# Performance work log

Hardware: AMD Instinct MI355X
Metric: run time of the kernel (lower is better)

The kernel has to match this reference:

```python
import jax, jax.numpy as jnp
import numpy as np

VOCAB = 10000
EMBED = 100
T = 80
UNITS = 512
B = 4096
RATE = 0.2  # Keras LSTMCell dropout on inputs, 4 gate masks, cached across timesteps


def setup_inputs() -> dict:
    key = jax.random.key(0)
    ks = jax.random.split(key, 10)
    s = 0.05
    return {
        "inputs": jax.random.randint(ks[0], (B, T), 0, VOCAB, dtype=jnp.int32),
        "embed": jax.random.normal(ks[1], (VOCAB, EMBED), dtype=jnp.float32) * s,
        "W0": jax.random.normal(ks[2], (EMBED, 4 * UNITS), dtype=jnp.float32) * s,
        "U0": jax.random.normal(ks[3], (UNITS, 4 * UNITS), dtype=jnp.float32) * s,
        "b0": jnp.zeros((4 * UNITS,), dtype=jnp.float32),
        "W1": jax.random.normal(ks[4], (UNITS, 4 * UNITS), dtype=jnp.float32) * s,
        "U1": jax.random.normal(ks[5], (UNITS, 4 * UNITS), dtype=jnp.float32) * s,
        "b1": jnp.zeros((4 * UNITS,), dtype=jnp.float32),
        "Wout": jax.random.normal(ks[6], (UNITS, 1), dtype=jnp.float32) * s,
        "bout": jnp.zeros((1,), dtype=jnp.float32),
    }


def _dropout_masks(key, shape):
    keep = 1.0 - RATE
    return jax.random.bernoulli(key, keep, shape).astype(jnp.float32) / keep


def _lstm_cell(h, c, xt, masks, W, U, b, in_dim):
    # masks: [4, B, in_dim] per-gate input dropout masks (fixed across time)
    # kernel layout: W.reshape(in_dim, 4, UNITS), gate order i, f, g(cand), o
    z = jnp.einsum('gbd,dgh->bgh', xt[None] * masks, W.reshape(in_dim, 4, UNITS))
    z = z + (h @ U + b).reshape(-1, 4, UNITS)
    i = jax.nn.sigmoid(z[:, 0])
    f = jax.nn.sigmoid(z[:, 1])
    g = jnp.tanh(z[:, 2])
    o = jax.nn.sigmoid(z[:, 3])
    c_new = f * c + i * g
    h_new = o * jnp.tanh(c_new)
    return h_new, c_new


def reference(inputs, embed, W0, U0, b0, W1, U1, b1, Wout, bout):
    x = embed[inputs]                      # [B, T, EMBED]
    mkey = jax.random.key(42)
    k0, k1 = jax.random.split(mkey)
    m0 = _dropout_masks(k0, (4, B, EMBED))
    m1 = _dropout_masks(k1, (4, B, UNITS))

    def step(carry, xt):
        h0, c0, h1, c1 = carry
        h0, c0 = _lstm_cell(h0, c0, xt, m0, W0, U0, b0, EMBED)
        h1, c1 = _lstm_cell(h1, c1, h0, m1, W1, U1, b1, UNITS)
        return (h0, c0, h1, c1), None

    init = tuple(jnp.zeros((B, UNITS), dtype=jnp.float32) for _ in range(4))
    (h0, c0, h1, c1), _ = jax.lax.scan(step, init, jnp.swapaxes(x, 0, 1))
    return jax.nn.sigmoid(h1 @ Wout + bout)   # [B, 1]
```

## Files before the change

### kernel.cpp

```cpp
#include <hip/hip_runtime.h>
#include <hip/hip_bf16.h>
#include <stdint.h>

#define BATCH 4096
#define TT    80
#define EMB   100
#define UNITS 512
#define N4    2048
#define K0P   128

typedef unsigned short ushort;
typedef unsigned char uchar;
typedef __bf16 bf16x8 __attribute__((ext_vector_type(8)));
typedef float f32x4 __attribute__((ext_vector_type(4)));

__device__ __forceinline__ uint32_t rotl32(uint32_t x, uint32_t r) {
  return (x << r) | (x >> (32u - r));
}
__device__ __forceinline__ void tf_round4(uint32_t& x0, uint32_t& x1,
                                          int r0, int r1, int r2, int r3) {
  x0 += x1; x1 = rotl32(x1, r0); x1 ^= x0;
  x0 += x1; x1 = rotl32(x1, r1); x1 ^= x0;
  x0 += x1; x1 = rotl32(x1, r2); x1 ^= x0;
  x0 += x1; x1 = rotl32(x1, r3); x1 ^= x0;
}
__device__ __forceinline__ void tf2x32(uint32_t k0, uint32_t k1,
                                       uint32_t x0, uint32_t x1,
                                       uint32_t& y0, uint32_t& y1) {
  uint32_t k2 = k0 ^ k1 ^ 0x1BD11BDAu;
  x0 += k0; x1 += k1;
  tf_round4(x0, x1, 13, 15, 26, 6);  x0 += k1; x1 += k2 + 1u;
  tf_round4(x0, x1, 17, 29, 16, 24); x0 += k2; x1 += k0 + 2u;
  tf_round4(x0, x1, 13, 15, 26, 6);  x0 += k0; x1 += k1 + 3u;
  tf_round4(x0, x1, 17, 29, 16, 24); x0 += k1; x1 += k2 + 4u;
  tf_round4(x0, x1, 13, 15, 26, 6);  x0 += k2; x1 += k0 + 5u;
  y0 = x0; y1 = x1;
}
__device__ __forceinline__ int keepbit(uint32_t u) {
  float f = __uint_as_float((u >> 9) | 0x3F800000u) - 1.0f;
  return f < 0.8f ? 1 : 0;
}

__device__ __forceinline__ ushort f2bf(float f) {
  uint32_t u = __float_as_uint(f);
  uint32_t r = (u + 0x7FFFu + ((u >> 16) & 1u)) >> 16;
  return (ushort)r;
}
__device__ __forceinline__ float bf2f(ushort u) {
  return __uint_as_float(((uint32_t)u) << 16);
}

#define M0N (4 * BATCH * EMB)
#define M1N (4 * BATCH * UNITS)

__global__ __launch_bounds__(256) void masks_kernel(uchar* __restrict__ m0p,
                                                    uchar* __restrict__ m1p) {
  uint32_t k0a, k0b, k1a, k1b;
  tf2x32(0u, 42u, 0u, 0u, k0a, k0b);
  tf2x32(0u, 42u, 0u, 1u, k1a, k1b);
  const int n0 = BATCH * EMB;
  const int n1 = BATCH * UNITS;
  const int total = n0 + n1;
  for (int i = blockIdx.x * blockDim.x + threadIdx.x; i < total;
       i += gridDim.x * blockDim.x) {
    if (i < n0) {
      uchar byte = 0;
#pragma unroll
      for (int g = 0; g < 4; g++) {
        uint32_t y0, y1;
        tf2x32(k0a, k0b, 0u, (uint32_t)(g * n0 + i), y0, y1);
        byte |= keepbit(y0 ^ y1) << g;
      }
      m0p[i] = byte;
    } else {
      int j = i - n0;
      uchar byte = 0;
#pragma unroll
      for (int g = 0; g < 4; g++) {
        uint32_t y0, y1;
        tf2x32(k1a, k1b, 0u, (uint32_t)(g * n1 + j), y0, y1);
        byte |= keepbit(y0 ^ y1) << g;
      }
      m1p[j] = byte;
    }
  }
}

__global__ __launch_bounds__(256) void convT(const float* __restrict__ src,
                                             ushort* __restrict__ dst,
                                             int Ksrc, int Kpad) {
  __shared__ float t[32][33];
  const int n0 = blockIdx.x * 32, kk0 = blockIdx.y * 32;
  const int tx = threadIdx.x & 31, ty = threadIdx.x >> 5;
#pragma unroll
  for (int r = ty; r < 32; r += 8) {
    const int k = kk0 + r;
    t[r][tx] = (k < Ksrc) ? src[(size_t)k * N4 + n0 + tx] : 0.f;
  }
  __syncthreads();
#pragma unroll
  for (int r = ty; r < 32; r += 8)
    dst[(size_t)(n0 + r) * Kpad + kk0 + tx] = f2bf(t[tx][r]);
}

__device__ __forceinline__ void xm0_prep_one(int i, int t,
                                             const int* __restrict__ inputs,
                                             const float* __restrict__ embed,
                                             const uchar* __restrict__ m0p,
                                             ushort* __restrict__ Xm0) {
  const int k = i & 127;
  const int b = (i >> 7) & 4095;
  const int g = i >> 19;
  float v = 0.f;
  if (k < EMB) {
    const int idx = inputs[b * TT + t];
    const float e = embed[(size_t)idx * EMB + k];
    v = ((m0p[b * EMB + k] >> g) & 1) ? e * 1.25f : 0.f;
  }
  Xm0[((size_t)g << 19) + (b << 7) + k] = f2bf(v);
}

__global__ __launch_bounds__(256) void prep0_kernel(const int* __restrict__ inputs,
                                                    const float* __restrict__ embed,
                                                    const uchar* __restrict__ m0p,
                                                    ushort* __restrict__ Xm0) {
  const int i = blockIdx.x * blockDim.x + threadIdx.x;
  xm0_prep_one(i, 0, inputs, embed, m0p, Xm0);
}

__device__ __forceinline__ void gload16(const void* g, void* l) {
  __builtin_amdgcn_global_load_lds(
      (const __attribute__((address_space(1))) unsigned int*)g,
      (__attribute__((address_space(3))) unsigned int*)l, 16, 0, 0);
}

__global__ __launch_bounds__(256) void cell_gemm_mfma(
    const ushort* __restrict__ A1, int K1,
    const ushort* __restrict__ B1,
    const ushort* __restrict__ A2,
    const ushort* __restrict__ B2,
    const float* __restrict__ bias,
    float* __restrict__ z) {
  __shared__ __align__(16) ushort As[128 * 32];
  __shared__ __align__(16) ushort Bs[128 * 32];

  const int tid = threadIdx.x;
  const int w = tid >> 6, l = tid & 63;
  const int bm0 = blockIdx.x * 128, bn0 = blockIdx.y * 128;
  const int gate = bn0 >> 9;
  const int wm = (w >> 1) * 64, wn = (w & 1) * 64;
  const int fr = l & 15, kq = l >> 4;
  const int schunk = (l & 3) * 8;
  const int srow_l = l >> 2;

  f32x4 acc[4][4] = {};

  const ushort* A1g = A1 + (size_t)gate * BATCH * K1;

#pragma unroll 1
  for (int seg = 0; seg < 2; seg++) {
    const ushort* A = seg ? A2 : A1g;
    const ushort* B = seg ? B2 : B1;
    const int K = seg ? UNITS : K1;
#pragma unroll 1
    for (int k0 = 0; k0 < K; k0 += 32) {
#pragma unroll
      for (int c2 = 0; c2 < 2; c2++) {
        const int r = (w * 2 + c2) * 16 + srow_l;
        gload16(A + (size_t)(bm0 + r) * K + k0 + schunk,
                (void*)(As + (w * 2 + c2) * 512));
        gload16(B + (size_t)(bn0 + r) * K + k0 + schunk,
                (void*)(Bs + (w * 2 + c2) * 512));
      }
      __syncthreads();
      bf16x8 a[4], b[4];
#pragma unroll
      for (int f = 0; f < 4; f++) {
        a[f] = *(const bf16x8*)&As[(wm + f * 16 + fr) * 32 + kq * 8];
        b[f] = *(const bf16x8*)&Bs[(wn + f * 16 + fr) * 32 + kq * 8];
      }
#pragma unroll
      for (int fi = 0; fi < 4; fi++)
#pragma unroll
        for (int fj = 0; fj < 4; fj++)
          acc[fi][fj] = __builtin_amdgcn_mfma_f32_16x16x32_bf16(
              a[fi], b[fj], acc[fi][fj], 0, 0, 0);
      __syncthreads();
    }
  }

#pragma unroll
  for (int fi = 0; fi < 4; fi++) {
#pragma unroll
    for (int fj = 0; fj < 4; fj++) {
      const int n = bn0 + wn + fj * 16 + fr;
      const float bv = bias[n];
#pragma unroll
      for (int j = 0; j < 4; j++) {
        const int m = bm0 + wm + fi * 16 + kq * 4 + j;
        z[(size_t)m * N4 + n] = acc[fi][fj][j] + bv;
      }
    }
  }
}

__global__ __launch_bounds__(256) void gates0_kernel(
    const float* __restrict__ z, float* __restrict__ c0,
    ushort* __restrict__ h0b, ushort* __restrict__ H0m,
    const uchar* __restrict__ m1p) {
  const int i = blockIdx.x * blockDim.x + threadIdx.x;
  const int b = i >> 9, h = i & 511;
  const float* zb = z + (size_t)b * N4;
  const float zi = zb[h], zf = zb[512 + h], zg = zb[1024 + h], zo = zb[1536 + h];
  const float iv = 1.f / (1.f + __expf(-zi));
  const float fv = 1.f / (1.f + __expf(-zf));
  const float gv = tanhf(zg);
  const float ov = 1.f / (1.f + __expf(-zo));
  const float cn = fv * c0[i] + iv * gv;
  c0[i] = cn;
  const float hn = ov * tanhf(cn);
  h0b[i] = f2bf(hn);
  const uchar mb = m1p[i];
  const float hm = hn * 1.25f;
#pragma unroll
  for (int g = 0; g < 4; g++)
    H0m[(size_t)g * (BATCH * UNITS) + i] = f2bf((mb >> g) & 1 ? hm : 0.f);
}

__global__ __launch_bounds__(256) void gates1_kernel(
    const float* __restrict__ z, float* __restrict__ c1,
    ushort* __restrict__ h1b,
    const int* __restrict__ inputs, const float* __restrict__ embed,
    const uchar* __restrict__ m0p, ushort* __restrict__ Xm0, int tnext) {
  const int i = blockIdx.x * blockDim.x + threadIdx.x;
  const int b = i >> 9, h = i & 511;
  const float* zb = z + (size_t)b * N4;
  const float zi = zb[h], zf = zb[512 + h], zg = zb[1024 + h], zo = zb[1536 + h];
  const float iv = 1.f / (1.f + __expf(-zi));
  const float fv = 1.f / (1.f + __expf(-zf));
  const float gv = tanhf(zg);
  const float ov = 1.f / (1.f + __expf(-zo));
  const float cn = fv * c1[i] + iv * gv;
  c1[i] = cn;
  h1b[i] = f2bf(ov * tanhf(cn));
  if (tnext < TT) xm0_prep_one(i, tnext, inputs, embed, m0p, Xm0);
}

__global__ __launch_bounds__(256) void out_kernel(const ushort* __restrict__ h1b,
                                                  const float* __restrict__ Wout,
                                                  const float* __restrict__ bout,
                                                  float* __restrict__ out) {
  const int wid = (blockIdx.x * blockDim.x + threadIdx.x) >> 6;
  const int lane = threadIdx.x & 63;
  if (wid >= BATCH) return;
  const ushort* hr = h1b + (size_t)wid * UNITS;
  float s = 0.f;
#pragma unroll
  for (int j = 0; j < UNITS; j += 64) s += bf2f(hr[j + lane]) * Wout[j + lane];
  for (int off = 32; off; off >>= 1) s += __shfl_down(s, off, 64);
  if (lane == 0) out[wid] = 1.f / (1.f + __expf(-(s + bout[0])));
}

extern "C" void kernel_launch(void* const* d_in, const int* in_sizes, int n_in,
                              void* d_out, int out_size, void* d_ws, size_t ws_size,
                              hipStream_t stream) {
  const int* inputs = (const int*)d_in[0];
  const float* embed = (const float*)d_in[1];
  const float* W0 = (const float*)d_in[2];
  const float* U0 = (const float*)d_in[3];
  const float* b0 = (const float*)d_in[4];
  const float* W1 = (const float*)d_in[5];
  const float* U1 = (const float*)d_in[6];
  const float* b1 = (const float*)d_in[7];
  const float* Wout = (const float*)d_in[8];
  const float* bout = (const float*)d_in[9];
  float* out = (float*)d_out;

  char* ws = (char*)d_ws;
  float* z    = (float*)(ws + 0);
  float* c0   = (float*)(ws + 33554432);
  float* c1   = (float*)(ws + 41943040);
  ushort* h0b = (ushort*)(ws + 50331648);
  ushort* h1b = (ushort*)(ws + 54525952);
  ushort* H0m = (ushort*)(ws + 58720256);
  ushort* Xm0 = (ushort*)(ws + 75497472);
  ushort* W0T = (ushort*)(ws + 79691776);
  ushort* U0T = (ushort*)(ws + 80216064);
  ushort* W1T = (ushort*)(ws + 82313216);
  ushort* U1T = (ushort*)(ws + 84410368);
  uchar* m0p  = (uchar*)(ws + 86507520);
  uchar* m1p  = (uchar*)(ws + 86917120);

  hipMemsetAsync(ws + 33554432, 0, 25165824, stream);

  masks_kernel<<<2048, 256, 0, stream>>>(m0p, m1p);

  {
    dim3 g0(N4 / 32, K0P / 32);
    convT<<<g0, 256, 0, stream>>>(W0, W0T, EMB, K0P);
    dim3 g1(N4 / 32, UNITS / 32);
    convT<<<g1, 256, 0, stream>>>(U0, U0T, UNITS, UNITS);
    convT<<<g1, 256, 0, stream>>>(W1, W1T, UNITS, UNITS);
    convT<<<g1, 256, 0, stream>>>(U1, U1T, UNITS, UNITS);
  }

  prep0_kernel<<<(4 * BATCH * K0P) / 256, 256, 0, stream>>>(inputs, embed, m0p, Xm0);

  const dim3 grid(BATCH / 128, N4 / 128);
  const int gblocks = (BATCH * UNITS) / 256;
  for (int t = 0; t < TT; t++) {
    cell_gemm_mfma<<<grid, 256, 0, stream>>>(Xm0, K0P, W0T, h0b, U0T, b0, z);
    gates0_kernel<<<gblocks, 256, 0, stream>>>(z, c0, h0b, H0m, m1p);
    cell_gemm_mfma<<<grid, 256, 0, stream>>>(H0m, UNITS, W1T, h1b, U1T, b1, z);
    gates1_kernel<<<gblocks, 256, 0, stream>>>(z, c1, h1b, inputs, embed, m0p,
                                               Xm0, t + 1);
  }

  out_kernel<<<BATCH * 64 / 256, 256, 0, stream>>>(h1b, Wout, bout, out);
}
```

Baseline: 6.032 ms.

## Fuse LSTM gemm and gate epilogue, pipeline both layers in one launch per step

Each per-timestep GEMM now computes all four gates for a 64-unit slice and applies the LSTM nonlinearity and cell update in its epilogue, so the fp32 z buffer and the separate gate kernels go away. Layer 1 at time t and layer 0 at time t+1 run as one launch using double-buffered h states, which halves the number of launches per step. Dropout masks are expanded to byte masks and applied with a bitwise AND on the bf16 A fragments in registers, and the 1.25 keep scale is folded into the transposed W weights, so the 4x masked copies of the inputs are no longer materialised. The cost is extra mask reads from global memory inside the GEMM loop and higher register pressure from a 4x8 accumulator tile.

```diff
diff --git a/kernel.cpp b/kernel.cpp
--- a/kernel.cpp
+++ b/kernel.cpp
@@ -6,13 +6,13 @@
 #define TT    80
 #define EMB   100
 #define UNITS 512
-#define N4    2048
 #define K0P   128
 
 typedef unsigned short ushort;
 typedef unsigned char uchar;
 typedef __bf16 bf16x8 __attribute__((ext_vector_type(8)));
 typedef float f32x4 __attribute__((ext_vector_type(4)));
+typedef uint32_t u32x4 __attribute__((ext_vector_type(4)));
 
 __device__ __forceinline__ uint32_t rotl32(uint32_t x, uint32_t r) {
   return (x << r) | (x >> (32u - r));
@@ -40,7 +40,6 @@
   float f = __uint_as_float((u >> 9) | 0x3F800000u) - 1.0f;
   return f < 0.8f ? 1 : 0;
 }
-
 __device__ __forceinline__ ushort f2bf(float f) {
   uint32_t u = __float_as_uint(f);
   uint32_t r = (u + 0x7FFFu + ((u >> 16) & 1u)) >> 16;
@@ -50,82 +49,68 @@
   return __uint_as_float(((uint32_t)u) << 16);
 }
 
-#define M0N (4 * BATCH * EMB)
-#define M1N (4 * BATCH * UNITS)
-
-__global__ __launch_bounds__(256) void masks_kernel(uchar* __restrict__ m0p,
-                                                    uchar* __restrict__ m1p) {
+__global__ __launch_bounds__(256) void masksB(uchar* __restrict__ m0B,
+                                              uchar* __restrict__ m1B) {
   uint32_t k0a, k0b, k1a, k1b;
   tf2x32(0u, 42u, 0u, 0u, k0a, k0b);
   tf2x32(0u, 42u, 0u, 1u, k1a, k1b);
-  const int n0 = BATCH * EMB;
-  const int n1 = BATCH * UNITS;
-  const int total = n0 + n1;
-  for (int i = blockIdx.x * blockDim.x + threadIdx.x; i < total;
+  const int T0 = 4 * BATCH * K0P;
+  const int T1 = 4 * BATCH * UNITS;
+  for (int i = blockIdx.x * blockDim.x + threadIdx.x; i < T0 + T1;
        i += gridDim.x * blockDim.x) {
-    if (i < n0) {
-      uchar byte = 0;
-#pragma unroll
-      for (int g = 0; g < 4; g++) {
+    if (i < T0) {
+      const int g = i >> 19, b = (i >> 7) & 4095, k = i & 127;
+      uchar v = 0;
+      if (k < EMB) {
         uint32_t y0, y1;
-        tf2x32(k0a, k0b, 0u, (uint32_t)(g * n0 + i), y0, y1);
-        byte |= keepbit(y0 ^ y1) << g;
+        tf2x32(k0a, k0b, 0u, (uint32_t)(g * (BATCH * EMB) + b * EMB + k), y0, y1);
+        v = keepbit(y0 ^ y1) ? 0xFFu : 0u;
       }
-      m0p[i] = byte;
+      m0B[i] = v;
     } else {
-      int j = i - n0;
-      uchar byte = 0;
-#pragma unroll
-      for (int g = 0; g < 4; g++) {
-        uint32_t y0, y1;
-        tf2x32(k1a, k1b, 0u, (uint32_t)(g * n1 + j), y0, y1);
-        byte |= keepbit(y0 ^ y1) << g;
-      }
-      m1p[j] = byte;
+      const int j = i - T0;
+      const int g = j >> 21, b = (j >> 9) & 4095, k = j & 511;
+      uint32_t y0, y1;
+      tf2x32(k1a, k1b, 0u, (uint32_t)(g * (BATCH * UNITS) + b * UNITS + k), y0, y1);
+      m1B[j] = keepbit(y0 ^ y1) ? 0xFFu : 0u;
     }
   }
 }
 
 __global__ __launch_bounds__(256) void convT(const float* __restrict__ src,
                                              ushort* __restrict__ dst,
-                                             int Ksrc, int Kpad) {
+                                             int Ksrc, int Kpad, float scale) {
   __shared__ float t[32][33];
   const int n0 = blockIdx.x * 32, kk0 = blockIdx.y * 32;
   const int tx = threadIdx.x & 31, ty = threadIdx.x >> 5;
 #pragma unroll
   for (int r = ty; r < 32; r += 8) {
     const int k = kk0 + r;
-    t[r][tx] = (k < Ksrc) ? src[(size_t)k * N4 + n0 + tx] : 0.f;
+    t[r][tx] = (k < Ksrc) ? src[(size_t)k * 2048 + n0 + tx] : 0.f;
   }
   __syncthreads();
 #pragma unroll
   for (int r = ty; r < 32; r += 8)
-    dst[(size_t)(n0 + r) * Kpad + kk0 + tx] = f2bf(t[tx][r]);
-}
-
-__device__ __forceinline__ void xm0_prep_one(int i, int t,
-                                             const int* __restrict__ inputs,
-                                             const float* __restrict__ embed,
-                                             const uchar* __restrict__ m0p,
-                                             ushort* __restrict__ Xm0) {
-  const int k = i & 127;
-  const int b = (i >> 7) & 4095;
-  const int g = i >> 19;
-  float v = 0.f;
-  if (k < EMB) {
-    const int idx = inputs[b * TT + t];
-    const float e = embed[(size_t)idx * EMB + k];
-    v = ((m0p[b * EMB + k] >> g) & 1) ? e * 1.25f : 0.f;
-  }
-  Xm0[((size_t)g << 19) + (b << 7) + k] = f2bf(v);
-}
-
-__global__ __launch_bounds__(256) void prep0_kernel(const int* __restrict__ inputs,
-                                                    const float* __restrict__ embed,
-                                                    const uchar* __restrict__ m0p,
-                                                    ushort* __restrict__ Xm0) {
-  const int i = blockIdx.x * blockDim.x + threadIdx.x;
-  xm0_prep_one(i, 0, inputs, embed, m0p, Xm0);
+    dst[(size_t)(n0 + r) * Kpad + kk0 + tx] = f2bf(scale * t[tx][r]);
+}
+
+__global__ __launch_bounds__(256) void xprep3(const int* __restrict__ inputs,
+                                              const float* __restrict__ embed,
+                                              ushort* __restrict__ X0,
+                                              ushort* __restrict__ X1,
+                                              ushort* __restrict__ X2) {
+  const int i = blockIdx.x * 256 + threadIdx.x;
+  const int s = i >> 16, r = i & 65535;
+  const int b = r >> 4, k = (r & 15) * 8;
+  ushort* X = (s == 0) ? X0 : (s == 1) ? X1 : X2;
+  const int idx = inputs[b * TT + s];
+  ushort v[8];
+#pragma unroll
+  for (int j = 0; j < 8; j++) {
+    const int kk = k + j;
+    v[j] = (kk < EMB) ? f2bf(embed[(size_t)idx * EMB + kk]) : (ushort)0;
+  }
+  *(bf16x8*)(X + (size_t)b * K0P + k) = *(bf16x8*)v;
 }
 
 __device__ __forceinline__ void gload16(const void* g, void* l) {
@@ -134,116 +119,185 @@
       (__attribute__((address_space(3))) unsigned int*)l, 16, 0, 0);
 }
 
-__global__ __launch_bounds__(256) void cell_gemm_mfma(
-    const ushort* __restrict__ A1, int K1,
-    const ushort* __restrict__ B1,
-    const ushort* __restrict__ A2,
-    const ushort* __restrict__ B2,
-    const float* __restrict__ bias,
-    float* __restrict__ z) {
-  __shared__ __align__(16) ushort As[128 * 32];
-  __shared__ __align__(16) ushort Bs[128 * 32];
-
-  const int tid = threadIdx.x;
+template <bool MASKED>
+__device__ __forceinline__ void gemm_seg(
+    const ushort* __restrict__ A, int K, const ushort* __restrict__ Bw,
+    const uchar* __restrict__ mB, int bm0, int bh0, int tid,
+    ushort* As, ushort* Bs, f32x4 acc[4][8]) {
   const int w = tid >> 6, l = tid & 63;
-  const int bm0 = blockIdx.x * 128, bn0 = blockIdx.y * 128;
-  const int gate = bn0 >> 9;
-  const int wm = (w >> 1) * 64, wn = (w & 1) * 64;
+  const int wr = w >> 1, wc = w & 1;
   const int fr = l & 15, kq = l >> 4;
-  const int schunk = (l & 3) * 8;
-  const int srow_l = l >> 2;
-
-  f32x4 acc[4][4] = {};
-
-  const ushort* A1g = A1 + (size_t)gate * BATCH * K1;
+  const int srow = l >> 2, schunk = (l & 3) * 8;
 
 #pragma unroll 1
-  for (int seg = 0; seg < 2; seg++) {
-    const ushort* A = seg ? A2 : A1g;
-    const ushort* B = seg ? B2 : B1;
-    const int K = seg ? UNITS : K1;
-#pragma unroll 1
-    for (int k0 = 0; k0 < K; k0 += 32) {
-#pragma unroll
-      for (int c2 = 0; c2 < 2; c2++) {
-        const int r = (w * 2 + c2) * 16 + srow_l;
-        gload16(A + (size_t)(bm0 + r) * K + k0 + schunk,
-                (void*)(As + (w * 2 + c2) * 512));
-        gload16(B + (size_t)(bn0 + r) * K + k0 + schunk,
-                (void*)(Bs + (w * 2 + c2) * 512));
+  for (int k0 = 0; k0 < K; k0 += 32) {
+#pragma unroll
+    for (int c2 = 0; c2 < 2; c2++) {
+      const int rt = w + c2 * 4;
+      gload16(A + (size_t)(bm0 + rt * 16 + srow) * K + k0 + schunk,
+              As + rt * 512);
+    }
+#pragma unroll
+    for (int c2 = 0; c2 < 4; c2++) {
+      const int ct = w * 4 + c2;
+      const int col = ct * 16 + srow;
+      const int nrow = (col >> 6) * 512 + bh0 + (col & 63);
+      gload16(Bw + (size_t)nrow * K + k0 + schunk, Bs + ct * 512);
+    }
+    uint2 md[4][4];
+    if (MASKED) {
+#pragma unroll
+      for (int fi = 0; fi < 4; fi++) {
+        const int row = bm0 + wr * 64 + fi * 16 + fr;
+#pragma unroll
+        for (int g = 0; g < 4; g++)
+          md[fi][g] = *(const uint2*)(mB + (size_t)(g * BATCH + row) * K + k0 +
+                                      kq * 8);
       }
-      __syncthreads();
-      bf16x8 a[4], b[4];
-#pragma unroll
-      for (int f = 0; f < 4; f++) {
-        a[f] = *(const bf16x8*)&As[(wm + f * 16 + fr) * 32 + kq * 8];
-        b[f] = *(const bf16x8*)&Bs[(wn + f * 16 + fr) * 32 + kq * 8];
+    }
+    __syncthreads();
+
+    u32x4 af[4];
+    bf16x8 bf[8];
+#pragma unroll
+    for (int fi = 0; fi < 4; fi++)
+      af[fi] = *(const u32x4*)&As[(wr * 64 + fi * 16 + fr) * 32 + kq * 8];
+#pragma unroll
+    for (int g = 0; g < 4; g++)
+#pragma unroll
+      for (int hf = 0; hf < 2; hf++)
+        bf[g * 2 + hf] =
+            *(const bf16x8*)&Bs[((g * 4 + wc * 2 + hf) * 16 + fr) * 32 + kq * 8];
+
+#pragma unroll
+    for (int g = 0; g < 4; g++) {
+#pragma unroll
+      for (int fi = 0; fi < 4; fi++) {
+        u32x4 ua = af[fi];
+        if (MASKED) {
+          const uint2 m = md[fi][g];
+          ua.x &= __builtin_amdgcn_perm(m.x, m.x, 0x01010000u);
+          ua.y &= __builtin_amdgcn_perm(m.x, m.x, 0x03030202u);
+          ua.z &= __builtin_amdgcn_perm(m.y, m.y, 0x01010000u);
+          ua.w &= __builtin_amdgcn_perm(m.y, m.y, 0x03030202u);
+        }
+        const bf16x8 a = __builtin_bit_cast(bf16x8, ua);
+        acc[fi][g * 2 + 0] = __builtin_amdgcn_mfma_f32_16x16x32_bf16(
+            a, bf[g * 2 + 0], acc[fi][g * 2 + 0], 0, 0, 0);
+        acc[fi][g * 2 + 1] = __builtin_amdgcn_mfma_f32_16x16x32_bf16(
+            a, bf[g * 2 + 1], acc[fi][g * 2 + 1], 0, 0, 0);
       }
-#pragma unroll
-      for (int fi = 0; fi < 4; fi++)
-#pragma unroll
-        for (int fj = 0; fj < 4; fj++)
-          acc[fi][fj] = __builtin_amdgcn_mfma_f32_16x16x32_bf16(
-              a[fi], b[fj], acc[fi][fj], 0, 0, 0);
-      __syncthreads();
-    }
-  }
-
+    }
+    __syncthreads();
+  }
+}
+
+__global__ __launch_bounds__(256, 2) void fused_step(
+    int nl1,
+    const ushort* __restrict__ h0b_cur, const ushort* __restrict__ h1b_prev,
+    ushort* __restrict__ h1b_out, float* __restrict__ c1f,
+    const ushort* __restrict__ W1T, const ushort* __restrict__ U1T,
+    const float* __restrict__ b1, int nl0, const ushort* __restrict__ Xcur,
+    ushort* __restrict__ h0b_out, float* __restrict__ c0f,
+    const ushort* __restrict__ W0T, const ushort* __restrict__ U0T,
+    const float* __restrict__ b0, const uchar* __restrict__ mask1B,
+    const uchar* __restrict__ mask0B, int tprep, const int* __restrict__ inputs,
+    const float* __restrict__ embed, ushort* __restrict__ Xprep) {
+  __shared__ __align__(16) ushort smem[12288];
+  const int bid = blockIdx.x, tid = threadIdx.x;
+  const bool isl1 = bid < nl1;
+  const int lbid = isl1 ? bid : bid - nl1;
+  const int cid = (lbid & 7) * 32 + (lbid >> 3);
+  const int bm0 = (cid >> 3) * 128;
+  const int bh0 = (cid & 7) * 64;
+  const int w = tid >> 6, l = tid & 63;
+  const int wr = w >> 1, wc = w & 1;
+  const int fr = l & 15, kq = l >> 4;
+
+  const ushort *Amask, *Aun, *BW, *BU;
+  const float* bias;
+  const uchar* mB;
+  float* cblob;
+  ushort* hout;
+  int Km;
+  if (isl1) {
+    Amask = h0b_cur; Km = UNITS; Aun = h1b_prev; BW = W1T; BU = U1T;
+    bias = b1; mB = mask1B; cblob = c1f; hout = h1b_out;
+  } else {
+    Amask = Xcur; Km = K0P; Aun = h0b_cur; BW = W0T; BU = U0T;
+    bias = b0; mB = mask0B; cblob = c0f; hout = h0b_out;
+  }
+
+  f32x4 acc[4][8] = {};
+  ushort* As = smem;
+  ushort* Bs = smem + 4096;
+
+  gemm_seg<true>(Amask, Km, BW, mB, bm0, bh0, tid, As, Bs, acc);
+  gemm_seg<false>(Aun, UNITS, BU, nullptr, bm0, bh0, tid, As, Bs, acc);
+
+  float* cb = cblob + (size_t)cid * 8192 + tid * 32;
+  f32x4 cold[8];
+#pragma unroll
+  for (int q = 0; q < 8; q++) cold[q] = *(const f32x4*)(cb + q * 4);
+
+  float bi[2], bfv[2], bg[2], bo[2];
+#pragma unroll
+  for (int hf = 0; hf < 2; hf++) {
+    const int h = bh0 + wc * 32 + hf * 16 + fr;
+    bi[hf] = bias[h];
+    bfv[hf] = bias[512 + h];
+    bg[hf] = bias[1024 + h];
+    bo[hf] = bias[1536 + h];
+  }
+
+  f32x4 cnew[8];
 #pragma unroll
   for (int fi = 0; fi < 4; fi++) {
 #pragma unroll
-    for (int fj = 0; fj < 4; fj++) {
-      const int n = bn0 + wn + fj * 16 + fr;
-      const float bv = bias[n];
-#pragma unroll
-      for (int j = 0; j < 4; j++) {
-        const int m = bm0 + wm + fi * 16 + kq * 4 + j;
-        z[(size_t)m * N4 + n] = acc[fi][fj][j] + bv;
+    for (int hf = 0; hf < 2; hf++) {
+#pragma unroll
+      for (int jj = 0; jj < 4; jj++) {
+        const float zi = acc[fi][0 + hf][jj] + bi[hf];
+        const float zf = acc[fi][2 + hf][jj] + bfv[hf];
+        const float zg = acc[fi][4 + hf][jj] + bg[hf];
+        const float zo = acc[fi][6 + hf][jj] + bo[hf];
+        const float iv = 1.f / (1.f + __expf(-zi));
+        const float fv = 1.f / (1.f + __expf(-zf));
+        const float gv = tanhf(zg);
+        const float ov = 1.f / (1.f + __expf(-zo));
+        const float cn = fv * cold[fi * 2 + hf][jj] + iv * gv;
+        cnew[fi * 2 + hf][jj] = cn;
+        const float hn = ov * tanhf(cn);
+        const int rloc = wr * 64 + fi * 16 + kq * 4 + jj;
+        const int hloc = wc * 32 + hf * 16 + fr;
+        smem[rloc * 64 + hloc] = f2bf(hn);
       }
     }
   }
-}
-
-__global__ __launch_bounds__(256) void gates0_kernel(
-    const float* __restrict__ z, float* __restrict__ c0,
-    ushort* __restrict__ h0b, ushort* __restrict__ H0m,
-    const uchar* __restrict__ m1p) {
-  const int i = blockIdx.x * blockDim.x + threadIdx.x;
-  const int b = i >> 9, h = i & 511;
-  const float* zb = z + (size_t)b * N4;
-  const float zi = zb[h], zf = zb[512 + h], zg = zb[1024 + h], zo = zb[1536 + h];
-  const float iv = 1.f / (1.f + __expf(-zi));
-  const float fv = 1.f / (1.f + __expf(-zf));
-  const float gv = tanhf(zg);
-  const float ov = 1.f / (1.f + __expf(-zo));
-  const float cn = fv * c0[i] + iv * gv;
-  c0[i] = cn;
-  const float hn = ov * tanhf(cn);
-  h0b[i] = f2bf(hn);
-  const uchar mb = m1p[i];
-  const float hm = hn * 1.25f;
-#pragma unroll
-  for (int g = 0; g < 4; g++)
-    H0m[(size_t)g * (BATCH * UNITS) + i] = f2bf((mb >> g) & 1 ? hm : 0.f);
-}
-
-__global__ __launch_bounds__(256) void gates1_kernel(
-    const float* __restrict__ z, float* __restrict__ c1,
-    ushort* __restrict__ h1b,
-    const int* __restrict__ inputs, const float* __restrict__ embed,
-    const uchar* __restrict__ m0p, ushort* __restrict__ Xm0, int tnext) {
-  const int i = blockIdx.x * blockDim.x + threadIdx.x;
-  const int b = i >> 9, h = i & 511;
-  const float* zb = z + (size_t)b * N4;
-  const float zi = zb[h], zf = zb[512 + h], zg = zb[1024 + h], zo = zb[1536 + h];
-  const float iv = 1.f / (1.f + __expf(-zi));
-  const float fv = 1.f / (1.f + __expf(-zf));
-  const float gv = tanhf(zg);
-  const float ov = 1.f / (1.f + __expf(-zo));
-  const float cn = fv * c1[i] + iv * gv;
-  c1[i] = cn;
-  h1b[i] = f2bf(ov * tanhf(cn));
-  if (tnext < TT) xm0_prep_one(i, tnext, inputs, embed, m0p, Xm0);
+#pragma unroll
+  for (int q = 0; q < 8; q++) *(f32x4*)(cb + q * 4) = cnew[q];
+  __syncthreads();
+
+#pragma unroll
+  for (int c2 = 0; c2 < 4; c2++) {
+    const int idx = c2 * 256 + tid;
+    const int rloc = idx >> 3, hcol = (idx & 7) * 8;
+    *(bf16x8*)(hout + (size_t)(bm0 + rloc) * UNITS + bh0 + hcol) =
+        *(const bf16x8*)&smem[rloc * 64 + hcol];
+  }
+
+  if (!isl1 && tprep >= 0) {
+    const int base = lbid * 2048 + tid * 8;
+    const int b = base >> 7, k = base & 127;
+    const int idx = inputs[b * TT + tprep];
+    ushort v[8];
+#pragma unroll
+    for (int j = 0; j < 8; j++) {
+      const int kk = k + j;
+      v[j] = (kk < EMB) ? f2bf(embed[(size_t)idx * EMB + kk]) : (ushort)0;
+    }
+    *(bf16x8*)(Xprep + (size_t)b * K0P + k) = *(bf16x8*)v;
+  }
 }
 
 __global__ __launch_bounds__(256) void out_kernel(const ushort* __restrict__ h1b,
@@ -277,44 +331,54 @@
   float* out = (float*)d_out;
 
   char* ws = (char*)d_ws;
-  float* z    = (float*)(ws + 0);
-  float* c0   = (float*)(ws + 33554432);
-  float* c1   = (float*)(ws + 41943040);
-  ushort* h0b = (ushort*)(ws + 50331648);
-  ushort* h1b = (ushort*)(ws + 54525952);
-  ushort* H0m = (ushort*)(ws + 58720256);
-  ushort* Xm0 = (ushort*)(ws + 75497472);
-  ushort* W0T = (ushort*)(ws + 79691776);
-  ushort* U0T = (ushort*)(ws + 80216064);
-  ushort* W1T = (ushort*)(ws + 82313216);
-  ushort* U1T = (ushort*)(ws + 84410368);
-  uchar* m0p  = (uchar*)(ws + 86507520);
-  uchar* m1p  = (uchar*)(ws + 86917120);
-
-  hipMemsetAsync(ws + 33554432, 0, 25165824, stream);
-
-  masks_kernel<<<2048, 256, 0, stream>>>(m0p, m1p);
-
+  const size_t MB = 1 << 20;
+  float* c0f    = (float*)(ws);
+  float* c1f    = (float*)(ws + 8 * MB);
+  ushort* h0b1  = (ushort*)(ws + 16 * MB);
+  ushort* h1b1  = (ushort*)(ws + 20 * MB);
+  ushort* h0b0  = (ushort*)(ws + 24 * MB);
+  ushort* h1b0  = (ushort*)(ws + 28 * MB);
+  ushort* X0    = (ushort*)(ws + 32 * MB);
+  ushort* X1    = (ushort*)(ws + 33 * MB);
+  ushort* X2    = (ushort*)(ws + 34 * MB);
+  ushort* W0T   = (ushort*)(ws + 35 * MB);
+  ushort* U0T   = (ushort*)(ws + 36 * MB);
+  ushort* W1T   = (ushort*)(ws + 38 * MB);
+  ushort* U1T   = (ushort*)(ws + 40 * MB);
+  uchar* m0B    = (uchar*)(ws + 42 * MB);
+  uchar* m1B    = (uchar*)(ws + 44 * MB);
+
+  ushort* h0b[2] = {h0b0, h0b1};
+  ushort* h1b[2] = {h1b0, h1b1};
+  ushort* X[3] = {X0, X1, X2};
+
+  hipMemsetAsync(ws, 0, 24 * MB, stream);
+
+  masksB<<<8192, 256, 0, stream>>>(m0B, m1B);
   {
-    dim3 g0(N4 / 32, K0P / 32);
-    convT<<<g0, 256, 0, stream>>>(W0, W0T, EMB, K0P);
-    dim3 g1(N4 / 32, UNITS / 32);
-    convT<<<g1, 256, 0, stream>>>(U0, U0T, UNITS, UNITS);
-    convT<<<g1, 256, 0, stream>>>(W1, W1T, UNITS, UNITS);
-    convT<<<g1, 256, 0, stream>>>(U1, U1T, UNITS, UNITS);
-  }
-
-  prep0_kernel<<<(4 * BATCH * K0P) / 256, 256, 0, stream>>>(inputs, embed, m0p, Xm0);
-
-  const dim3 grid(BATCH / 128, N4 / 128);
-  const int gblocks = (BATCH * UNITS) / 256;
-  for (int t = 0; t < TT; t++) {
-    cell_gemm_mfma<<<grid, 256, 0, stream>>>(Xm0, K0P, W0T, h0b, U0T, b0, z);
-    gates0_kernel<<<gblocks, 256, 0, stream>>>(z, c0, h0b, H0m, m1p);
-    cell_gemm_mfma<<<grid, 256, 0, stream>>>(H0m, UNITS, W1T, h1b, U1T, b1, z);
-    gates1_kernel<<<gblocks, 256, 0, stream>>>(z, c1, h1b, inputs, embed, m0p,
-                                               Xm0, t + 1);
-  }
-
-  out_kernel<<<BATCH * 64 / 256, 256, 0, stream>>>(h1b, Wout, bout, out);
-}
+    dim3 g0(2048 / 32, K0P / 32);
+    convT<<<g0, 256, 0, stream>>>(W0, W0T, EMB, K0P, 1.25f);
+    dim3 g1(2048 / 32, UNITS / 32);
+    convT<<<g1, 256, 0, stream>>>(U0, U0T, UNITS, UNITS, 1.0f);
+    convT<<<g1, 256, 0, stream>>>(W1, W1T, UNITS, UNITS, 1.25f);
+    convT<<<g1, 256, 0, stream>>>(U1, U1T, UNITS, UNITS, 1.0f);
+  }
+  xprep3<<<768, 256, 0, stream>>>(inputs, embed, X0, X1, X2);
+
+  fused_step<<<256, 256, 0, stream>>>(
+      0, h0b[1], h1b[1], h1b[0], c1f, W1T, U1T, b1,
+      256, X[0], h0b[0], c0f, W0T, U0T, b0, m1B, m0B,
+      -1, inputs, embed, X[0]);
+
+  for (int k = 0; k < TT; k++) {
+    const int p = k & 1;
+    const int nl0 = (k < TT - 1) ? 256 : 0;
+    const int tprep = (k + 3 < TT) ? (k + 3) : -1;
+    fused_step<<<256 + nl0, 256, 0, stream>>>(
+        256, h0b[p], h1b[p ^ 1], h1b[p], c1f, W1T, U1T, b1,
+        nl0, X[(k + 1) % 3], h0b[p ^ 1], c0f, W0T, U0T, b0, m1B, m0B,
+        tprep, inputs, embed, X[k % 3]);
+  }
+
+  out_kernel<<<BATCH * 64 / 256, 256, 0, stream>>>(h1b[1], Wout, bout, out);
+}
```

New measurement: 6.276 ms. +4.1%, slower.
